# Performance work log

Measured on AMD Instinct MI355X. Metric: run time of the kernel, lower is better.

The kernel has to match this reference:

```python
import jax, jax.numpy as jnp
import numpy as np

B, N, C, DFF, NH, KNN = 4, 2048, 256, 1024, 4, 16


def _gelu(x):
    return jax.nn.gelu(x, approximate=False)  # torch nn.GELU default = exact erf


def _ln(x, g, b, eps=1e-5):
    m = jnp.mean(x, axis=-1, keepdims=True)
    v = jnp.mean((x - m) ** 2, axis=-1, keepdims=True)
    return (x - m) * jax.lax.rsqrt(v + eps) * g + b


def setup_inputs() -> dict:
    key = jax.random.key(0)
    ks = jax.random.split(key, 16)
    w = lambda k, shp: jax.random.normal(k, shp, jnp.float32) * 0.02
    return {
        "src1": jax.random.normal(ks[0], (B, C, N), jnp.float32),
        "src2": jax.random.normal(ks[1], (B, C, N), jnp.float32),
        "pos": jax.random.uniform(ks[2], (B, 3, N), jnp.float32),
        # input_proj Conv1d(C, C, 1)
        "Wp": w(ks[3], (C, C)), "bp": jnp.zeros((C,), jnp.float32),
        # rel_pos_encoder: Conv2d(3, C//4, 1) -> GELU -> Conv2d(C//4, 1, 1)
        "Wr1": w(ks[4], (C // 4, 3)), "br1": jnp.zeros((C // 4,), jnp.float32),
        "Wr2": w(ks[5], (1, C // 4)), "br2": jnp.zeros((1,), jnp.float32),
        # MultiheadAttention packed in-proj + out-proj
        "Wqkv": w(ks[6], (3 * C, C)), "bqkv": jnp.zeros((3 * C,), jnp.float32),
        "Wo": w(ks[7], (C, C)), "bo": jnp.zeros((C,), jnp.float32),
        # norms
        "g13": jnp.ones((C,), jnp.float32), "b13": jnp.zeros((C,), jnp.float32),
        "g12": jnp.ones((C,), jnp.float32), "b12": jnp.zeros((C,), jnp.float32),
        # FFN
        "W1": w(ks[8], (DFF, C)), "b1": jnp.zeros((DFF,), jnp.float32),
        "W2": w(ks[9], (C, DFF)), "b2": jnp.zeros((C,), jnp.float32),
    }


def reference(src1, src2, pos, Wp, bp, Wr1, br1, Wr2, br2, Wqkv, bqkv,
              Wo, bo, g13, b13, g12, b12, W1, b1, W2, b2):
    b, _, n = src1.shape
    c = Wp.shape[0]
    h = NH
    dh = c // h

    # input_proj (1x1 conv == matmul over channel dim); go to (b, n, c)
    s1 = jnp.einsum('oc,bcn->bno', Wp, src1) + bp
    s2 = jnp.einsum('oc,bcn->bno', Wp, src2) + bp

    # --- KNN + rel-pos bias ---
    p = pos.transpose(0, 2, 1)  # (b, n, 3)
    sq = jnp.sum(p * p, axis=-1)  # (b, n)
    dist = sq[:, :, None] + sq[:, None, :] - 2.0 * jnp.einsum('bnd,bmd->bnm', p, p)
    _, idx = jax.lax.top_k(-dist, KNN)  # (b, n, KNN) nearest (incl. self)
    knn_pos = jax.vmap(lambda pp, ii: pp[ii])(p, idx)  # (b, n, KNN, 3)
    rel = p[:, :, None, :] - knn_pos  # (b, n, KNN, 3)
    hid = _gelu(jnp.einsum('bnkd,od->bnko', rel, Wr1) + br1)
    bias_vals = (jnp.einsum('bnko,uo->bnku', hid, Wr2) + br2)[..., 0]  # (b, n, KNN)

    attn_bias = jnp.full((b, n, n), -jnp.inf, dtype=s1.dtype)
    bi = jnp.arange(b)[:, None, None]
    ri = jnp.arange(n)[None, :, None]
    attn_bias = attn_bias.at[bi, ri, idx].set(bias_vals)  # scatter along dim 2

    # --- pre-norm (norm13 shared for q and kv) ---
    x1 = _ln(s1, g13, b13)
    x2 = _ln(s2, g13, b13)

    # --- multihead attention with additive float mask ---
    Wq, Wk, Wv = jnp.split(Wqkv, 3, axis=0)
    bq, bk, bv = jnp.split(bqkv, 3)
    q = (x1 @ Wq.T + bq).reshape(b, n, h, dh)
    k = (x2 @ Wk.T + bk).reshape(b, n, h, dh)
    v = (x2 @ Wv.T + bv).reshape(b, n, h, dh)
    scores = jnp.einsum('bqhd,bkhd->bhqk', q, k) / jnp.sqrt(jnp.asarray(dh, s1.dtype))
    scores = scores + attn_bias[:, None, :, :]  # repeat_interleave(nhead) == head broadcast
    attn = jax.nn.softmax(scores, axis=-1)
    o = jnp.einsum('bhqk,bkhd->bqhd', attn, v).reshape(b, n, c) @ Wo.T + bo

    x1 = _ln(x1 + o, g12, b12)
    ff = _gelu(x1 @ W1.T + b1) @ W2.T + b2
    out = x1 + ff
    return out.transpose(0, 2, 1)  # (b, c, n)
```

## Files before the change

kernel.cpp:

```cpp
#include <hip/hip_runtime.h>
#include <hip/hip_bf16.h>
#include <math.h>

constexpr int kB = 4;
constexpr int kN = 2048;
constexpr int kC = 256;
constexpr int kDFF = 1024;
constexpr int kKNN = 16;
constexpr int kDH = 64;

typedef __attribute__((ext_vector_type(8))) short short8;
typedef __attribute__((ext_vector_type(4))) float float4v;

__device__ __forceinline__ float gelu_erf(float x) {
    return 0.5f * x * (1.0f + erff(x * 0.70710678118654752440f));
}

__device__ __forceinline__ short f2b(float f) {
    unsigned u = __float_as_uint(f);
    u = u + 0x7FFFu + ((u >> 16) & 1u);
    return (short)(u >> 16);
}

__device__ __forceinline__ float b2f(short h) {
    unsigned u = ((unsigned)(unsigned short)h) << 16;
    return __uint_as_float(u);
}

__global__ __launch_bounds__(256) void cvt_weights(
    const float* __restrict__ Wqkv, const float* __restrict__ Wo,
    const float* __restrict__ W1, const float* __restrict__ W2,
    short* __restrict__ dst)
{
    const int i = (blockIdx.x * 256 + threadIdx.x) * 8;
    const float* src; int off;
    if (i < 196608)      { src = Wqkv; off = i; }
    else if (i < 262144) { src = Wo;   off = i - 196608; }
    else if (i < 524288) { src = W1;   off = i - 262144; }
    else                 { src = W2;   off = i - 524288; }
    short8 v;
    #pragma unroll
    for (int j = 0; j < 8; j++) v[j] = f2b(src[off + j]);
    *(short8*)&dst[i] = v;
}

__global__ __launch_bounds__(256) void cvt_wp(
    const float* __restrict__ Wp, short* __restrict__ hi, short* __restrict__ lo)
{
    const int i = (blockIdx.x * 256 + threadIdx.x) * 8;
    short8 h, l;
    #pragma unroll
    for (int j = 0; j < 8; j++) {
        float v = Wp[i + j];
        short hh = f2b(v);
        h[j] = hh;
        l[j] = f2b(v - b2f(hh));
    }
    *(short8*)&hi[i] = h;
    *(short8*)&lo[i] = l;
}

__global__ __launch_bounds__(256) void transpose_cvt(
    const float* __restrict__ src1, const float* __restrict__ src2,
    short* __restrict__ hiT, short* __restrict__ loT)
{
    __shared__ float tile[32][33];
    const int z = blockIdx.z;
    const float* in = (z < 4 ? src1 : src2) + (size_t)(z & 3) * kC * kN;
    const int n0 = blockIdx.x * 32;
    const int c0 = blockIdx.y * 32;
    const int tx = threadIdx.x;
    const int ty = threadIdx.y;
    #pragma unroll
    for (int i = 0; i < 32; i += 8)
        tile[ty + i][tx] = in[(size_t)(c0 + ty + i) * kN + (n0 + tx)];
    __syncthreads();
    #pragma unroll
    for (int i = 0; i < 32; i += 8) {
        float v = tile[tx][ty + i];
        short h = f2b(v);
        short l = f2b(v - b2f(h));
        size_t o = ((size_t)z * kN + (n0 + ty + i)) * kC + (c0 + tx);
        hiT[o] = h;
        loT[o] = l;
    }
}

__global__ __launch_bounds__(256) void proj_mfma(
    const short* __restrict__ Ahi, const short* __restrict__ Alo,
    const short* __restrict__ Whi, const short* __restrict__ Wlo,
    const float* __restrict__ bias, float* __restrict__ out)
{
    __shared__ __align__(16) short AsmH[64][40], AsmL[64][40];
    __shared__ __align__(16) short BsmH[64][40], BsmL[64][40];

    const int tid = threadIdx.x;
    const int n0 = blockIdx.x * 64;
    const size_t m0 = (size_t)blockIdx.y * 64;
    const int lane = tid & 63, wv = tid >> 6;
    const int lm = lane & 15, quad = lane >> 4;
    const int r = tid >> 2, q = tid & 3;

    float4v acc[4] = {};

    for (int k0 = 0; k0 < kC; k0 += 32) {
        *(short8*)&AsmH[r][q * 8] = *(const short8*)&Ahi[(m0 + r) * kC + k0 + q * 8];
        *(short8*)&AsmL[r][q * 8] = *(const short8*)&Alo[(m0 + r) * kC + k0 + q * 8];
        *(short8*)&BsmH[r][q * 8] = *(const short8*)&Whi[(size_t)(n0 + r) * kC + k0 + q * 8];
        *(short8*)&BsmL[r][q * 8] = *(const short8*)&Wlo[(size_t)(n0 + r) * kC + k0 + q * 8];
        __syncthreads();

        short8 ah = *(const short8*)&AsmH[wv * 16 + lm][quad * 8];
        short8 al = *(const short8*)&AsmL[wv * 16 + lm][quad * 8];
        #pragma unroll
        for (int j4 = 0; j4 < 4; j4++) {
            short8 bh = *(const short8*)&BsmH[j4 * 16 + lm][quad * 8];
            short8 bl = *(const short8*)&BsmL[j4 * 16 + lm][quad * 8];
            acc[j4] = __builtin_amdgcn_mfma_f32_16x16x32_bf16(al, bh, acc[j4], 0, 0, 0);
            acc[j4] = __builtin_amdgcn_mfma_f32_16x16x32_bf16(ah, bl, acc[j4], 0, 0, 0);
            acc[j4] = __builtin_amdgcn_mfma_f32_16x16x32_bf16(ah, bh, acc[j4], 0, 0, 0);
        }
        __syncthreads();
    }

    #pragma unroll
    for (int j4 = 0; j4 < 4; j4++) {
        const int n = n0 + j4 * 16 + lm;
        const float bn = bias[n];
        #pragma unroll
        for (int rg = 0; rg < 4; rg++) {
            const size_t m = m0 + wv * 16 + quad * 4 + rg;
            out[m * kC + n] = acc[j4][rg] + bn;
        }
    }
}

__global__ __launch_bounds__(256) void mfma_gemm_bf(
    const short* __restrict__ A, const short* __restrict__ W,
    const float* __restrict__ bias, const float* __restrict__ resid,
    float* __restrict__ out, short* __restrict__ outbf,
    int M, int Nout, int K, int epi)
{
    __shared__ __align__(16) short Asm[64][40];
    __shared__ __align__(16) short Bsm[64][40];

    const int tid = threadIdx.x;
    const int n0 = blockIdx.x * 64;
    const int m0 = blockIdx.y * 64;
    const int lane = tid & 63, wv = tid >> 6;
    const int lm = lane & 15, quad = lane >> 4;
    const int r = tid >> 2, q = tid & 3;

    float4v acc[4] = {};

    for (int k0 = 0; k0 < K; k0 += 32) {
        *(short8*)&Asm[r][q * 8] = *(const short8*)&A[(size_t)(m0 + r) * K + k0 + q * 8];
        *(short8*)&Bsm[r][q * 8] = *(const short8*)&W[(size_t)(n0 + r) * K + k0 + q * 8];
        __syncthreads();

        short8 af = *(const short8*)&Asm[wv * 16 + lm][quad * 8];
        #pragma unroll
        for (int j4 = 0; j4 < 4; j4++) {
            short8 bf = *(const short8*)&Bsm[j4 * 16 + lm][quad * 8];
            acc[j4] = __builtin_amdgcn_mfma_f32_16x16x32_bf16(af, bf, acc[j4], 0, 0, 0);
        }
        __syncthreads();
    }

    #pragma unroll
    for (int j4 = 0; j4 < 4; j4++) {
        const int n = n0 + j4 * 16 + lm;
        const float bn = bias[n];
        #pragma unroll
        for (int rg = 0; rg < 4; rg++) {
            const int m = m0 + wv * 16 + quad * 4 + rg;
            float v = acc[j4][rg] + bn;
            if (resid) v += resid[(size_t)m * Nout + n];
            if (epi == 1) v = gelu_erf(v);
            if (out)   out[(size_t)m * Nout + n] = v;
            if (outbf) outbf[(size_t)m * Nout + n] = f2b(v);
        }
    }
}

__global__ __launch_bounds__(256) void qkv_gemm(
    const short* __restrict__ x1bf, const short* __restrict__ x2bf,
    const short* __restrict__ Wqkvbf, const float* __restrict__ bqkv,
    float* __restrict__ qb, float* __restrict__ kvb)
{
    __shared__ __align__(16) short Asm[64][40];
    __shared__ __align__(16) short Bsm[64][40];

    const int n0g = blockIdx.x * 64;
    const int m0 = blockIdx.y * 64;
    const short* A; float* out; int Nout; int ncol0;
    if (n0g < 256) { A = x1bf; out = qb;  Nout = 256; ncol0 = n0g; }
    else           { A = x2bf; out = kvb; Nout = 512; ncol0 = n0g - 256; }

    const int tid = threadIdx.x;
    const int lane = tid & 63, wv = tid >> 6;
    const int lm = lane & 15, quad = lane >> 4;
    const int r = tid >> 2, q = tid & 3;

    float4v acc[4] = {};

    for (int k0 = 0; k0 < kC; k0 += 32) {
        *(short8*)&Asm[r][q * 8] = *(const short8*)&A[(size_t)(m0 + r) * kC + k0 + q * 8];
        *(short8*)&Bsm[r][q * 8] = *(const short8*)&Wqkvbf[(size_t)(n0g + r) * kC + k0 + q * 8];
        __syncthreads();

        short8 af = *(const short8*)&Asm[wv * 16 + lm][quad * 8];
        #pragma unroll
        for (int j4 = 0; j4 < 4; j4++) {
            short8 bf = *(const short8*)&Bsm[j4 * 16 + lm][quad * 8];
            acc[j4] = __builtin_amdgcn_mfma_f32_16x16x32_bf16(af, bf, acc[j4], 0, 0, 0);
        }
        __syncthreads();
    }

    #pragma unroll
    for (int j4 = 0; j4 < 4; j4++) {
        const int nc = ncol0 + j4 * 16 + lm;
        const float bn = bqkv[n0g + j4 * 16 + lm];
        #pragma unroll
        for (int rg = 0; rg < 4; rg++) {
            const int m = m0 + wv * 16 + quad * 4 + rg;
            out[(size_t)m * Nout + nc] = acc[j4][rg] + bn;
        }
    }
}

__global__ __launch_bounds__(256) void ln_kernel(
    float* __restrict__ x, short* __restrict__ xbf,
    const float* __restrict__ g, const float* __restrict__ bb)
{
    const size_t row = blockIdx.x;
    const int t = threadIdx.x;
    float v = x[row * kC + t];

    __shared__ float red4[4];
    float s = v;
    #pragma unroll
    for (int off = 32; off; off >>= 1) s += __shfl_xor(s, off, 64);
    if ((t & 63) == 0) red4[t >> 6] = s;
    __syncthreads();
    float mean = (red4[0] + red4[1] + red4[2] + red4[3]) * (1.0f / kC);

    float d = v - mean;
    float s2 = d * d;
    #pragma unroll
    for (int off = 32; off; off >>= 1) s2 += __shfl_xor(s2, off, 64);
    __syncthreads();
    if ((t & 63) == 0) red4[t >> 6] = s2;
    __syncthreads();
    float var = (red4[0] + red4[1] + red4[2] + red4[3]) * (1.0f / kC);

    float r = 1.0f / sqrtf(var + 1e-5f);
    float o = d * r * g[t] + bb[t];
    x[row * kC + t] = o;
    xbf[row * kC + t] = f2b(o);
}

#define KNN_RESCAN(CH, BM, BI)                                        \
    do {                                                              \
        float nb_ = 1e30f; int ni_ = kN;                              \
        _Pragma("unroll")                                             \
        for (int c8_ = 0; c8_ < 8; c8_++) {                           \
            int c_ = (CH) * 8 + c8_;                                  \
            float dd_ = (mask & (1u << c_)) ? 1e30f : cd[c_];         \
            if (dd_ < nb_) { nb_ = dd_; ni_ = c_ * 64 + lane; }       \
        }                                                             \
        BM = nb_; BI = ni_;                                           \
    } while (0)

__global__ __launch_bounds__(256) void knn_kernel(
    const float* __restrict__ pos,
    const float* __restrict__ Wr1, const float* __restrict__ br1,
    const float* __restrict__ Wr2, const float* __restrict__ br2,
    int* __restrict__ idx_out, float* __restrict__ bias_out)
{
    __shared__ float px[kN], py[kN], pz[kN];
    __shared__ int selS[4][kKNN];

    const int b = blockIdx.y;
    const int t = threadIdx.x;
    const int lane = t & 63, wv = t >> 6;
    const int n = blockIdx.x * 4 + wv;

    const float* pb = pos + (size_t)b * 3 * kN;
    for (int m = t; m < kN; m += 256) {
        px[m] = pb[m]; py[m] = pb[kN + m]; pz[m] = pb[2 * kN + m];
    }
    __syncthreads();

    const float qx = px[n], qy = py[n], qz = pz[n];
    const float qsq = __fadd_rn(__fadd_rn(__fmul_rn(qx, qx), __fmul_rn(qy, qy)),
                                __fmul_rn(qz, qz));

    float cd[32];
    float bm0 = 1e30f, bm1 = 1e30f, bm2 = 1e30f, bm3 = 1e30f;
    int bi0 = kN, bi1 = kN, bi2 = kN, bi3 = kN;
    #pragma unroll
    for (int c8 = 0; c8 < 8; c8++) {
        {
            const int c = c8, m = c * 64 + lane;
            float ax = px[m], ay = py[m], az = pz[m];
            float asq = __fadd_rn(__fadd_rn(__fmul_rn(ax, ax), __fmul_rn(ay, ay)), __fmul_rn(az, az));
            float dot = __fadd_rn(__fadd_rn(__fmul_rn(qx, ax), __fmul_rn(qy, ay)), __fmul_rn(qz, az));
            float d = __fsub_rn(__fadd_rn(qsq, asq), __fmul_rn(2.0f, dot));
            cd[c] = d;
            if (d < bm0) { bm0 = d; bi0 = m; }
        }
        {
            const int c = c8 + 8, m = c * 64 + lane;
            float ax = px[m], ay = py[m], az = pz[m];
            float asq = __fadd_rn(__fadd_rn(__fmul_rn(ax, ax), __fmul_rn(ay, ay)), __fmul_rn(az, az));
            float dot = __fadd_rn(__fadd_rn(__fmul_rn(qx, ax), __fmul_rn(qy, ay)), __fmul_rn(qz, az));
            float d = __fsub_rn(__fadd_rn(qsq, asq), __fmul_rn(2.0f, dot));
            cd[c] = d;
            if (d < bm1) { bm1 = d; bi1 = m; }
        }
        {
            const int c = c8 + 16, m = c * 64 + lane;
            float ax = px[m], ay = py[m], az = pz[m];
            float asq = __fadd_rn(__fadd_rn(__fmul_rn(ax, ax), __fmul_rn(ay, ay)), __fmul_rn(az, az));
            float dot = __fadd_rn(__fadd_rn(__fmul_rn(qx, ax), __fmul_rn(qy, ay)), __fmul_rn(qz, az));
            float d = __fsub_rn(__fadd_rn(qsq, asq), __fmul_rn(2.0f, dot));
            cd[c] = d;
            if (d < bm2) { bm2 = d; bi2 = m; }
        }
        {
            const int c = c8 + 24, m = c * 64 + lane;
            float ax = px[m], ay = py[m], az = pz[m];
            float asq = __fadd_rn(__fadd_rn(__fmul_rn(ax, ax), __fmul_rn(ay, ay)), __fmul_rn(az, az));
            float dot = __fadd_rn(__fadd_rn(__fmul_rn(qx, ax), __fmul_rn(qy, ay)), __fmul_rn(qz, az));
            float d = __fsub_rn(__fadd_rn(qsq, asq), __fmul_rn(2.0f, dot));
            cd[c] = d;
            if (d < bm3) { bm3 = d; bi3 = m; }
        }
    }

    unsigned mask = 0;
    for (int r = 0; r < kKNN; r++) {
        float best = bm0; int bid = bi0;
        if (bm1 < best) { best = bm1; bid = bi1; }
        if (bm2 < best) { best = bm2; bid = bi2; }
        if (bm3 < best) { best = bm3; bid = bi3; }

        #pragma unroll
        for (int off = 1; off < 64; off <<= 1) {
            float od = __shfl_xor(best, off, 64);
            int   oi = __shfl_xor(bid, off, 64);
            if (od < best || (od == best && oi < bid)) { best = od; bid = oi; }
        }
        if (lane == 0) selS[wv][r] = bid;
        if ((bid & 63) == lane) mask |= 1u << (bid >> 6);

        if (r < kKNN - 1) {
            const int sch = __builtin_amdgcn_readfirstlane(bid >> 9);
            switch (sch) {
                case 0:  KNN_RESCAN(0, bm0, bi0); break;
                case 1:  KNN_RESCAN(1, bm1, bi1); break;
                case 2:  KNN_RESCAN(2, bm2, bi2); break;
                default: KNN_RESCAN(3, bm3, bi3); break;
            }
        }
    }

    const int k = lane >> 2;
    const int part = lane & 3;
    const int m = selS[wv][k];
    const float rx = qx - px[m], ry = qy - py[m], rz = qz - pz[m];
    float partial = 0.0f;
    #pragma unroll
    for (int jj = 0; jj < 16; jj++) {
        int o = part * 16 + jj;
        float h = rx * Wr1[o * 3 + 0] + ry * Wr1[o * 3 + 1] +
                  rz * Wr1[o * 3 + 2] + br1[o];
        partial += gelu_erf(h) * Wr2[o];
    }
    partial += __shfl_xor(partial, 1, 64);
    partial += __shfl_xor(partial, 2, 64);
    if (part == 0) {
        size_t o = ((size_t)b * kN + n) * kKNN + k;
        idx_out[o] = m;
        bias_out[o] = partial + br2[0];
    }
}

__global__ __launch_bounds__(256) void attn_kernel(
    const float* __restrict__ q, const float* __restrict__ kv,
    const int* __restrict__ idx, const float* __restrict__ bias,
    short* __restrict__ obf)
{
    const int n = blockIdx.x;
    const int b = blockIdx.y;
    const int t = threadIdx.x;
    const int h = t >> 6;
    const int d = t & 63;

    const size_t row = (size_t)b * kN + n;
    const float qv = q[row * kC + h * kDH + d];

    __shared__ int   sidx[kKNN];
    __shared__ float sb[kKNN];
    if (t < kKNN) { sidx[t] = idx[row * kKNN + t]; sb[t] = bias[row * kKNN + t]; }
    __syncthreads();

    float sc[kKNN];
    #pragma unroll
    for (int j = 0; j < kKNN; j++) {
        size_t kr = (size_t)b * kN + sidx[j];
        float p = qv * kv[kr * 512 + h * kDH + d];
        #pragma unroll
        for (int off = 32; off; off >>= 1) p += __shfl_xor(p, off, 64);
        sc[j] = p * 0.125f + sb[j];
    }
    float mx = sc[0];
    #pragma unroll
    for (int j = 1; j < kKNN; j++) mx = fmaxf(mx, sc[j]);
    float den = 0.0f;
    #pragma unroll
    for (int j = 0; j < kKNN; j++) { sc[j] = expf(sc[j] - mx); den += sc[j]; }
    const float inv = 1.0f / den;
    float o = 0.0f;
    #pragma unroll
    for (int j = 0; j < kKNN; j++) {
        size_t kr = (size_t)b * kN + sidx[j];
        o += sc[j] * inv * kv[kr * 512 + kC + h * kDH + d];
    }
    obf[row * kC + h * kDH + d] = f2b(o);
}

__global__ __launch_bounds__(256) void transpose_f32(
    const float* __restrict__ z, float* __restrict__ out)
{
    __shared__ float tile[32][33];
    const int b = blockIdx.z;
    const int n0 = blockIdx.x * 32;
    const int c0 = blockIdx.y * 32;
    const int tx = threadIdx.x;
    const int ty = threadIdx.y;
    #pragma unroll
    for (int i = 0; i < 32; i += 8)
        tile[ty + i][tx] = z[(size_t)b * kN * kC + (size_t)(n0 + ty + i) * kC + (c0 + tx)];
    __syncthreads();
    #pragma unroll
    for (int i = 0; i < 32; i += 8)
        out[(size_t)b * kC * kN + (size_t)(c0 + ty + i) * kN + (n0 + tx)] =
            tile[tx][ty + i];
}

extern "C" void kernel_launch(void* const* d_in, const int* in_sizes, int n_in,
                              void* d_out, int out_size, void* d_ws, size_t ws_size,
                              hipStream_t stream)
{
    const float* src1 = (const float*)d_in[0];
    const float* src2 = (const float*)d_in[1];
    const float* pos  = (const float*)d_in[2];
    const float* Wp   = (const float*)d_in[3];
    const float* bp   = (const float*)d_in[4];
    const float* Wr1  = (const float*)d_in[5];
    const float* br1  = (const float*)d_in[6];
    const float* Wr2  = (const float*)d_in[7];
    const float* br2  = (const float*)d_in[8];
    const float* Wqkv = (const float*)d_in[9];
    const float* bqkv = (const float*)d_in[10];
    const float* Wo   = (const float*)d_in[11];
    const float* bo   = (const float*)d_in[12];
    const float* g13  = (const float*)d_in[13];
    const float* b13  = (const float*)d_in[14];
    const float* g12  = (const float*)d_in[15];
    const float* b12  = (const float*)d_in[16];
    const float* W1   = (const float*)d_in[17];
    const float* b1   = (const float*)d_in[18];
    const float* W2   = (const float*)d_in[19];
    const float* b2   = (const float*)d_in[20];
    float* out = (float*)d_out;

    const size_t S = (size_t)kB * kN * kC;
    float* ws = (float*)d_ws;
    float* x1  = ws;
    float* s2  = ws + S;
    float* qb  = ws + 2 * S;
    float* kvb = ws + 3 * S;
    float* yb  = ws + 2 * S;
    float* zb  = ws + S;
    short* srcThi = (short*)(ws + 2 * S);
    short* srcTlo = (short*)(ws + 3 * S);
    short* x1bf = (short*)(ws + 5 * S);
    short* x2bf = (short*)(ws + 5 * S) + S;
    short* ybf  = (short*)(ws + 6 * S);
    short* obf  = (short*)(ws + 6 * S) + S;
    short* hbf  = (short*)(ws + 3 * S);
    int*   idxb  = (int*)(ws + 7 * S);
    float* biasb = ws + 7 * S + (size_t)kB * kN * kKNN;
    short* wbf    = (short*)(ws + 7 * S + 2 * (size_t)kB * kN * kKNN);
    short* Wqkvbf = wbf;
    short* Wobf   = wbf + 196608;
    short* W1bf   = wbf + 262144;
    short* W2bf   = wbf + 524288;
    short* Wphi   = wbf + 786432;
    short* Wplo   = wbf + 851968;

    const int M = kB * kN;

    cvt_weights<<<384, 256, 0, stream>>>(Wqkv, Wo, W1, W2, wbf);
    cvt_wp<<<32, 256, 0, stream>>>(Wp, Wphi, Wplo);

    transpose_cvt<<<dim3(kN / 32, kC / 32, 8), dim3(32, 8), 0, stream>>>(
        src1, src2, srcThi, srcTlo);
    proj_mfma<<<dim3(kC / 64, 2 * M / 64), 256, 0, stream>>>(
        srcThi, srcTlo, Wphi, Wplo, bp, x1);

    ln_kernel<<<2 * M, 256, 0, stream>>>(x1, x1bf, g13, b13);

    knn_kernel<<<dim3(kN / 4, kB), 256, 0, stream>>>(pos, Wr1, br1, Wr2, br2, idxb, biasb);

    qkv_gemm<<<dim3(12, M / 64), 256, 0, stream>>>(x1bf, x2bf, Wqkvbf, bqkv, qb, kvb);

    attn_kernel<<<dim3(kN, kB), 256, 0, stream>>>(qb, kvb, idxb, biasb, obf);

    mfma_gemm_bf<<<dim3(kC / 64, M / 64), 256, 0, stream>>>(
        obf, Wobf, bo, x1, yb, nullptr, M, kC, kC, 0);
    ln_kernel<<<M, 256, 0, stream>>>(yb, ybf, g12, b12);

    mfma_gemm_bf<<<dim3(kDFF / 64, M / 64), 256, 0, stream>>>(
        ybf, W1bf, b1, nullptr, nullptr, hbf, M, kDFF, kC, 1);
    mfma_gemm_bf<<<dim3(kC / 64, M / 64), 256, 0, stream>>>(
        hbf, W2bf, b2, yb, zb, nullptr, M, kC, kDFF, 0);

    transpose_f32<<<dim3(kN / 32, kC / 32, kB), dim3(32, 8), 0, stream>>>(zb, out);
}
```

Baseline: 304.5 us.

## Process two KNN queries per wavefront and use 512-thread blocks

Each wavefront in the KNN kernel now handles two query points. Candidate coordinates and their squared norms are loaded once from LDS and reused for both queries, and the block grows to 8 waves (16 queries), so the per-block LDS fill of all positions is amortized over four times as many queries. In exchange, register pressure roughly doubles (two 32-entry distance arrays) and there are four times fewer blocks, which may reduce occupancy or cause spills.

```diff
diff --git a/kernel.cpp b/kernel.cpp
--- a/kernel.cpp
+++ b/kernel.cpp
@@ -261,130 +261,126 @@
     xbf[row * kC + t] = f2b(o);
 }
 
-#define KNN_RESCAN(CH, BM, BI)                                        \
+#define KNN_RESCAN2(QI, CH)                                           \
     do {                                                              \
         float nb_ = 1e30f; int ni_ = kN;                              \
         _Pragma("unroll")                                             \
         for (int c8_ = 0; c8_ < 8; c8_++) {                           \
             int c_ = (CH) * 8 + c8_;                                  \
-            float dd_ = (mask & (1u << c_)) ? 1e30f : cd[c_];         \
+            float dd_ = (mask[QI] & (1u << c_)) ? 1e30f : cd[QI][c_]; \
             if (dd_ < nb_) { nb_ = dd_; ni_ = c_ * 64 + lane; }       \
         }                                                             \
-        BM = nb_; BI = ni_;                                           \
+        bm[QI][CH] = nb_; bi[QI][CH] = ni_;                           \
     } while (0)
 
-__global__ __launch_bounds__(256) void knn_kernel(
+__global__ __launch_bounds__(512) void knn_kernel(
     const float* __restrict__ pos,
     const float* __restrict__ Wr1, const float* __restrict__ br1,
     const float* __restrict__ Wr2, const float* __restrict__ br2,
     int* __restrict__ idx_out, float* __restrict__ bias_out)
 {
     __shared__ float px[kN], py[kN], pz[kN];
-    __shared__ int selS[4][kKNN];
+    __shared__ int selS[8][2][kKNN];
 
     const int b = blockIdx.y;
     const int t = threadIdx.x;
     const int lane = t & 63, wv = t >> 6;
-    const int n = blockIdx.x * 4 + wv;
+    const int nq0 = blockIdx.x * 16 + wv * 2;
 
     const float* pb = pos + (size_t)b * 3 * kN;
-    for (int m = t; m < kN; m += 256) {
+    for (int m = t; m < kN; m += 512) {
         px[m] = pb[m]; py[m] = pb[kN + m]; pz[m] = pb[2 * kN + m];
     }
     __syncthreads();
 
-    const float qx = px[n], qy = py[n], qz = pz[n];
-    const float qsq = __fadd_rn(__fadd_rn(__fmul_rn(qx, qx), __fmul_rn(qy, qy)),
-                                __fmul_rn(qz, qz));
-
-    float cd[32];
-    float bm0 = 1e30f, bm1 = 1e30f, bm2 = 1e30f, bm3 = 1e30f;
-    int bi0 = kN, bi1 = kN, bi2 = kN, bi3 = kN;
+    float qx[2], qy[2], qz[2], qsq[2];
+    #pragma unroll
+    for (int qi = 0; qi < 2; qi++) {
+        qx[qi] = px[nq0 + qi]; qy[qi] = py[nq0 + qi]; qz[qi] = pz[nq0 + qi];
+        qsq[qi] = __fadd_rn(__fadd_rn(__fmul_rn(qx[qi], qx[qi]), __fmul_rn(qy[qi], qy[qi])),
+                            __fmul_rn(qz[qi], qz[qi]));
+    }
+
+    float cd[2][32];
+    float bm[2][4];
+    int bi[2][4];
+    #pragma unroll
+    for (int qi = 0; qi < 2; qi++)
+        #pragma unroll
+        for (int ch = 0; ch < 4; ch++) { bm[qi][ch] = 1e30f; bi[qi][ch] = kN; }
+
     #pragma unroll
     for (int c8 = 0; c8 < 8; c8++) {
-        {
-            const int c = c8, m = c * 64 + lane;
+        #pragma unroll
+        for (int ch = 0; ch < 4; ch++) {
+            const int c = ch * 8 + c8;
+            const int m = c * 64 + lane;
             float ax = px[m], ay = py[m], az = pz[m];
-            float asq = __fadd_rn(__fadd_rn(__fmul_rn(ax, ax), __fmul_rn(ay, ay)), __fmul_rn(az, az));
-            float dot = __fadd_rn(__fadd_rn(__fmul_rn(qx, ax), __fmul_rn(qy, ay)), __fmul_rn(qz, az));
-            float d = __fsub_rn(__fadd_rn(qsq, asq), __fmul_rn(2.0f, dot));
-            cd[c] = d;
-            if (d < bm0) { bm0 = d; bi0 = m; }
-        }
-        {
-            const int c = c8 + 8, m = c * 64 + lane;
-            float ax = px[m], ay = py[m], az = pz[m];
-            float asq = __fadd_rn(__fadd_rn(__fmul_rn(ax, ax), __fmul_rn(ay, ay)), __fmul_rn(az, az));
-            float dot = __fadd_rn(__fadd_rn(__fmul_rn(qx, ax), __fmul_rn(qy, ay)), __fmul_rn(qz, az));
-            float d = __fsub_rn(__fadd_rn(qsq, asq), __fmul_rn(2.0f, dot));
-            cd[c] = d;
-            if (d < bm1) { bm1 = d; bi1 = m; }
-        }
-        {
-            const int c = c8 + 16, m = c * 64 + lane;
-            float ax = px[m], ay = py[m], az = pz[m];
-            float asq = __fadd_rn(__fadd_rn(__fmul_rn(ax, ax), __fmul_rn(ay, ay)), __fmul_rn(az, az));
-            float dot = __fadd_rn(__fadd_rn(__fmul_rn(qx, ax), __fmul_rn(qy, ay)), __fmul_rn(qz, az));
-            float d = __fsub_rn(__fadd_rn(qsq, asq), __fmul_rn(2.0f, dot));
-            cd[c] = d;
-            if (d < bm2) { bm2 = d; bi2 = m; }
-        }
-        {
-            const int c = c8 + 24, m = c * 64 + lane;
-            float ax = px[m], ay = py[m], az = pz[m];
-            float asq = __fadd_rn(__fadd_rn(__fmul_rn(ax, ax), __fmul_rn(ay, ay)), __fmul_rn(az, az));
-            float dot = __fadd_rn(__fadd_rn(__fmul_rn(qx, ax), __fmul_rn(qy, ay)), __fmul_rn(qz, az));
-            float d = __fsub_rn(__fadd_rn(qsq, asq), __fmul_rn(2.0f, dot));
-            cd[c] = d;
-            if (d < bm3) { bm3 = d; bi3 = m; }
-        }
-    }
-
-    unsigned mask = 0;
+            float asq = __fadd_rn(__fadd_rn(__fmul_rn(ax, ax), __fmul_rn(ay, ay)),
+                                  __fmul_rn(az, az));
+            #pragma unroll
+            for (int qi = 0; qi < 2; qi++) {
+                float dot = __fadd_rn(__fadd_rn(__fmul_rn(qx[qi], ax), __fmul_rn(qy[qi], ay)),
+                                      __fmul_rn(qz[qi], az));
+                float d = __fsub_rn(__fadd_rn(qsq[qi], asq), __fmul_rn(2.0f, dot));
+                cd[qi][c] = d;
+                if (d < bm[qi][ch]) { bm[qi][ch] = d; bi[qi][ch] = m; }
+            }
+        }
+    }
+
+    unsigned mask[2] = {0u, 0u};
     for (int r = 0; r < kKNN; r++) {
-        float best = bm0; int bid = bi0;
-        if (bm1 < best) { best = bm1; bid = bi1; }
-        if (bm2 < best) { best = bm2; bid = bi2; }
-        if (bm3 < best) { best = bm3; bid = bi3; }
-
-        #pragma unroll
-        for (int off = 1; off < 64; off <<= 1) {
-            float od = __shfl_xor(best, off, 64);
-            int   oi = __shfl_xor(bid, off, 64);
-            if (od < best || (od == best && oi < bid)) { best = od; bid = oi; }
-        }
-        if (lane == 0) selS[wv][r] = bid;
-        if ((bid & 63) == lane) mask |= 1u << (bid >> 6);
-
-        if (r < kKNN - 1) {
-            const int sch = __builtin_amdgcn_readfirstlane(bid >> 9);
-            switch (sch) {
-                case 0:  KNN_RESCAN(0, bm0, bi0); break;
-                case 1:  KNN_RESCAN(1, bm1, bi1); break;
-                case 2:  KNN_RESCAN(2, bm2, bi2); break;
-                default: KNN_RESCAN(3, bm3, bi3); break;
+        #pragma unroll
+        for (int qi = 0; qi < 2; qi++) {
+            float best = bm[qi][0]; int bid = bi[qi][0];
+            if (bm[qi][1] < best) { best = bm[qi][1]; bid = bi[qi][1]; }
+            if (bm[qi][2] < best) { best = bm[qi][2]; bid = bi[qi][2]; }
+            if (bm[qi][3] < best) { best = bm[qi][3]; bid = bi[qi][3]; }
+
+            #pragma unroll
+            for (int off = 1; off < 64; off <<= 1) {
+                float od = __shfl_xor(best, off, 64);
+                int   oi = __shfl_xor(bid, off, 64);
+                if (od < best || (od == best && oi < bid)) { best = od; bid = oi; }
+            }
+            if (lane == 0) selS[wv][qi][r] = bid;
+            if ((bid & 63) == lane) mask[qi] |= 1u << (bid >> 6);
+
+            if (r < kKNN - 1) {
+                const int sch = __builtin_amdgcn_readfirstlane(bid >> 9);
+                switch (sch) {
+                    case 0:  KNN_RESCAN2(qi, 0); break;
+                    case 1:  KNN_RESCAN2(qi, 1); break;
+                    case 2:  KNN_RESCAN2(qi, 2); break;
+                    default: KNN_RESCAN2(qi, 3); break;
+                }
             }
         }
     }
 
     const int k = lane >> 2;
     const int part = lane & 3;
-    const int m = selS[wv][k];
-    const float rx = qx - px[m], ry = qy - py[m], rz = qz - pz[m];
-    float partial = 0.0f;
-    #pragma unroll
-    for (int jj = 0; jj < 16; jj++) {
-        int o = part * 16 + jj;
-        float h = rx * Wr1[o * 3 + 0] + ry * Wr1[o * 3 + 1] +
-                  rz * Wr1[o * 3 + 2] + br1[o];
-        partial += gelu_erf(h) * Wr2[o];
-    }
-    partial += __shfl_xor(partial, 1, 64);
-    partial += __shfl_xor(partial, 2, 64);
-    if (part == 0) {
-        size_t o = ((size_t)b * kN + n) * kKNN + k;
-        idx_out[o] = m;
-        bias_out[o] = partial + br2[0];
+    #pragma unroll
+    for (int qi = 0; qi < 2; qi++) {
+        const int n = nq0 + qi;
+        const int m = selS[wv][qi][k];
+        const float rx = qx[qi] - px[m], ry = qy[qi] - py[m], rz = qz[qi] - pz[m];
+        float partial = 0.0f;
+        #pragma unroll
+        for (int jj = 0; jj < 16; jj++) {
+            int o = part * 16 + jj;
+            float h = rx * Wr1[o * 3 + 0] + ry * Wr1[o * 3 + 1] +
+                      rz * Wr1[o * 3 + 2] + br1[o];
+            partial += gelu_erf(h) * Wr2[o];
+        }
+        partial += __shfl_xor(partial, 1, 64);
+        partial += __shfl_xor(partial, 2, 64);
+        if (part == 0) {
+            size_t o = ((size_t)b * kN + n) * kKNN + k;
+            idx_out[o] = m;
+            bias_out[o] = partial + br2[0];
+        }
     }
 }
 
@@ -515,7 +511,7 @@
 
     ln_kernel<<<2 * M, 256, 0, stream>>>(x1, x1bf, g13, b13);
 
-    knn_kernel<<<dim3(kN / 4, kB), 256, 0, stream>>>(pos, Wr1, br1, Wr2, br2, idxb, biasb);
+    knn_kernel<<<dim3(kN / 16, kB), 512, 0, stream>>>(pos, Wr1, br1, Wr2, br2, idxb, biasb);
 
     qkv_gemm<<<dim3(12, M / 64), 256, 0, stream>>>(x1bf, x2bf, Wqkvbf, bqkv, qb, kvb);
 
```

New measurement: 324.7 us. 6.6% more time.
